# Kernel tuning notes

Hardware: AMD Instinct MI355X
Metric: run time of the kernel (lower is better)

The kernel has to match this reference:

```python
import jax, jax.numpy as jnp
import numpy as np

NUM_NODES = 100000
EMB_DIM = 256
HID_DIM = 256
NUM_REL = 500
NUM_EDGES = 250000


def setup_inputs() -> dict:
    key = jax.random.key(0)
    ks = jax.random.split(key, 6)
    x = jax.random.normal(ks[0], (NUM_NODES, EMB_DIM), dtype=jnp.float32)
    edge_index = jax.random.randint(ks[1], (2, NUM_EDGES), 0, NUM_NODES, dtype=jnp.int64)
    edge_type = jax.random.randint(ks[2], (NUM_EDGES,), 0, NUM_REL, dtype=jnp.int64)
    # nn.Linear weights: shape [out, in]; _init_weights -> normal(0,1), bias zero
    W_head = jax.random.normal(ks[3], (HID_DIM, EMB_DIM), dtype=jnp.float32)
    b_head = jnp.zeros((HID_DIM,), dtype=jnp.float32)
    W_tail = jax.random.normal(ks[4], (HID_DIM, EMB_DIM), dtype=jnp.float32)
    b_tail = jnp.zeros((HID_DIM,), dtype=jnp.float32)
    rel_emb = jax.random.normal(ks[5], (NUM_REL, HID_DIM), dtype=jnp.float32)
    return {"x": x, "edge_index": edge_index, "edge_type": edge_type,
            "W_head": W_head, "b_head": b_head,
            "W_tail": W_tail, "b_tail": b_tail, "rel_emb": rel_emb}


def reference(x, edge_index, edge_type, W_head, b_head, W_tail, b_tail, rel_emb):
    # gcn == 'no' branch of DistMultNet.forward
    h_head = x[edge_index[0]] @ W_head.T + b_head          # [E, H]
    h_tail = x[edge_index[1]] @ W_tail.T + b_tail          # [E, H]
    h_rel = rel_emb[edge_type]                             # [E, H]
    scores = jnp.sum(h_head * h_rel * h_tail, axis=1)      # [E]
    return jax.nn.sigmoid(scores)
```

## Files before the change

kernel.cpp:

```cpp
#include <hip/hip_runtime.h>
#include <math.h>

#define EMB 256

typedef _Float16 half8 __attribute__((ext_vector_type(8)));
typedef _Float16 half4v __attribute__((ext_vector_type(4)));
typedef float f32x4 __attribute__((ext_vector_type(4)));

__device__ __forceinline__ void split2(const float4 v, half4v& hi, half4v& lo) {
    hi[0] = (_Float16)v.x; hi[1] = (_Float16)v.y;
    hi[2] = (_Float16)v.z; hi[3] = (_Float16)v.w;
    lo[0] = (_Float16)(v.x - (float)hi[0]);
    lo[1] = (_Float16)(v.y - (float)hi[1]);
    lo[2] = (_Float16)(v.z - (float)hi[2]);
    lo[3] = (_Float16)(v.w - (float)hi[3]);
}

__global__ __launch_bounds__(256, 2)
void gemm_split_mfma(const float* __restrict__ X,
                     const float* __restrict__ Wh, const float* __restrict__ bh,
                     const float* __restrict__ Wt, const float* __restrict__ bt,
                     float* __restrict__ Hout, float* __restrict__ Tout, int M)
{
    __shared__ __align__(16) _Float16 Ab[128 * 64];
    __shared__ __align__(16) _Float16 Bb[128 * 64];

    const int tid = threadIdx.x;
    const int sel = blockIdx.x >> 1;
    const int n0  = (blockIdx.x & 1) << 7;
    const int m0  = blockIdx.y << 7;
    const float* __restrict__ Wsel = sel ? Wt : Wh;
    const float* __restrict__ bsel = sel ? bt : bh;
    float* __restrict__ OUT = sel ? Tout : Hout;

    const int lane = tid & 63;
    const int wv = tid >> 6;
    const int wm = (wv >> 1) << 6;
    const int wn = (wv & 1) << 6;
    const int l15 = lane & 15, l4 = lane >> 4;

    const int q    = tid & 7;
    const int srow = tid >> 3;
    const int ghi  = q >> 1;
    const int wby  = (q & 1) << 3;

    f32x4 acc[4][4];
#pragma unroll
    for (int i = 0; i < 4; ++i)
#pragma unroll
        for (int j = 0; j < 4; ++j) acc[i][j] = (f32x4){0.f, 0.f, 0.f, 0.f};

    float4 xg[4], wg[4];
#pragma unroll
    for (int p = 0; p < 4; ++p) {
        const int r = srow + p * 32;
        const int gm = m0 + r;
        xg[p] = (gm < M) ? *(const float4*)&X[(size_t)gm * EMB + q * 4]
                         : make_float4(0.f, 0.f, 0.f, 0.f);
        wg[p] = *(const float4*)&Wsel[(size_t)(n0 + r) * EMB + q * 4];
    }

    for (int k0 = 0; k0 < EMB; k0 += 32) {
        __syncthreads();
#pragma unroll
        for (int p = 0; p < 4; ++p) {
            const int r = srow + p * 32;
            const int r7 = r & 7;
            half4v hi, lo;
            split2(xg[p], hi, lo);
            char* abase = (char*)Ab + r * 128 + wby;
            *(half4v*)(abase + (((ghi    ) ^ r7) << 4)) = hi;
            *(half4v*)(abase + (((ghi + 4) ^ r7) << 4)) = lo;
            split2(wg[p], hi, lo);
            char* bbase = (char*)Bb + r * 128 + wby;
            *(half4v*)(bbase + (((ghi    ) ^ r7) << 4)) = hi;
            *(half4v*)(bbase + (((ghi + 4) ^ r7) << 4)) = lo;
        }
        __syncthreads();

        if (k0 + 32 < EMB) {
            const int kn = k0 + 32 + q * 4;
#pragma unroll
            for (int p = 0; p < 4; ++p) {
                const int r = srow + p * 32;
                const int gm = m0 + r;
                xg[p] = (gm < M) ? *(const float4*)&X[(size_t)gm * EMB + kn]
                                 : make_float4(0.f, 0.f, 0.f, 0.f);
                wg[p] = *(const float4*)&Wsel[(size_t)(n0 + r) * EMB + kn];
            }
        }

        half8 ah[4], al[4];
#pragma unroll
        for (int f = 0; f < 4; ++f) {
            const int m = wm + f * 16 + l15;
            const char* arow = (const char*)Ab + m * 128;
            ah[f] = *(const half8*)(arow + (((l4    ) ^ (m & 7)) << 4));
            al[f] = *(const half8*)(arow + (((l4 + 4) ^ (m & 7)) << 4));
        }
#pragma unroll
        for (int j = 0; j < 4; ++j) {
            const int n = wn + j * 16 + l15;
            const char* brow = (const char*)Bb + n * 128;
            const half8 bhv = *(const half8*)(brow + (((l4    ) ^ (n & 7)) << 4));
            const half8 blv = *(const half8*)(brow + (((l4 + 4) ^ (n & 7)) << 4));
#pragma unroll
            for (int i = 0; i < 4; ++i) {
                acc[i][j] = __builtin_amdgcn_mfma_f32_16x16x32_f16(ah[i], bhv, acc[i][j], 0, 0, 0);
                acc[i][j] = __builtin_amdgcn_mfma_f32_16x16x32_f16(ah[i], blv, acc[i][j], 0, 0, 0);
                acc[i][j] = __builtin_amdgcn_mfma_f32_16x16x32_f16(al[i], bhv, acc[i][j], 0, 0, 0);
            }
        }
    }

#pragma unroll
    for (int i = 0; i < 4; ++i) {
        const int rbase = m0 + wm + i * 16 + l4 * 4;
#pragma unroll
        for (int rg = 0; rg < 4; ++rg) {
            const int gr = rbase + rg;
            if (gr < M) {
                float* dst = &OUT[(size_t)gr * EMB + n0 + wn];
#pragma unroll
                for (int j = 0; j < 4; ++j) {
                    const int col = j * 16 + l15;
                    dst[col] = acc[i][j][rg] + bsel[n0 + wn + col];
                }
            }
        }
    }
}

__global__ __launch_bounds__(256)
void edge_score(const float* __restrict__ H, const float* __restrict__ T,
                const float* __restrict__ rel, const int* __restrict__ ei,
                const int* __restrict__ et, float* __restrict__ out, int E)
{
    const int lane = threadIdx.x & 63;
    const int wid = threadIdx.x >> 6;
    const int e = blockIdx.x * 4 + wid;
    if (e >= E) return;

    const int src = ei[e];
    const int dst = ei[E + e];
    const int r = et[e];

    const float4 h = *(const float4*)&H[(size_t)src * EMB + lane * 4];
    const float4 t = *(const float4*)&T[(size_t)dst * EMB + lane * 4];
    const float4 g = *(const float4*)&rel[(size_t)r * EMB + lane * 4];

    float s = h.x * g.x * t.x + h.y * g.y * t.y + h.z * g.z * t.z + h.w * g.w * t.w;
#pragma unroll
    for (int off = 32; off > 0; off >>= 1)
        s += __shfl_xor(s, off, 64);

    if (lane == 0) out[e] = 1.0f / (1.0f + expf(-s));
}

__global__ __launch_bounds__(256)
void edge_direct(const float* __restrict__ X, const int* __restrict__ ei,
                 const int* __restrict__ et,
                 const float* __restrict__ Wh, const float* __restrict__ bh,
                 const float* __restrict__ Wt, const float* __restrict__ bt,
                 const float* __restrict__ rel, float* __restrict__ out, int E)
{
    __shared__ float xsrc[EMB], xdst[EMB];
    __shared__ float red[256];
    const int e = blockIdx.x;
    const int tid = threadIdx.x;
    const int src = ei[e], dst = ei[E + e], r = et[e];

    xsrc[tid] = X[(size_t)src * EMB + tid];
    xdst[tid] = X[(size_t)dst * EMB + tid];
    __syncthreads();

    float ah = 0.f, at = 0.f;
    const float* wh = Wh + (size_t)tid * EMB;
    const float* wt = Wt + (size_t)tid * EMB;
#pragma unroll 8
    for (int k = 0; k < EMB; k += 4) {
        float4 w4 = *(const float4*)&wh[k];
        ah += w4.x * xsrc[k] + w4.y * xsrc[k + 1] + w4.z * xsrc[k + 2] + w4.w * xsrc[k + 3];
        float4 v4 = *(const float4*)&wt[k];
        at += v4.x * xdst[k] + v4.y * xdst[k + 1] + v4.z * xdst[k + 2] + v4.w * xdst[k + 3];
    }
    red[tid] = (ah + bh[tid]) * rel[(size_t)r * EMB + tid] * (at + bt[tid]);
    __syncthreads();
    for (int s2 = 128; s2 > 0; s2 >>= 1) {
        if (tid < s2) red[tid] += red[tid + s2];
        __syncthreads();
    }
    if (tid == 0) out[e] = 1.0f / (1.0f + expf(-red[0]));
}

extern "C" void kernel_launch(void* const* d_in, const int* in_sizes, int n_in,
                              void* d_out, int out_size, void* d_ws, size_t ws_size,
                              hipStream_t stream) {
    const float* x   = (const float*)d_in[0];
    const int*   ei  = (const int*)d_in[1];
    const int*   et  = (const int*)d_in[2];
    const float* Wh  = (const float*)d_in[3];
    const float* bh  = (const float*)d_in[4];
    const float* Wt  = (const float*)d_in[5];
    const float* bt  = (const float*)d_in[6];
    const float* rel = (const float*)d_in[7];
    float* out = (float*)d_out;

    const int M = in_sizes[0] / EMB;
    const int E = in_sizes[2];

    const size_t need = (size_t)2 * M * EMB * sizeof(float);
    if (ws_size >= need) {
        float* H = (float*)d_ws;
        float* T = H + (size_t)M * EMB;
        dim3 grid(4, (M + 127) / 128);
        gemm_split_mfma<<<grid, 256, 0, stream>>>(x, Wh, bh, Wt, bt, H, T, M);
        edge_score<<<(E + 3) / 4, 256, 0, stream>>>(H, T, rel, ei, et, out, E);
    } else {
        edge_direct<<<E, 256, 0, stream>>>(x, ei, et, Wh, bh, Wt, bt, rel, out, E);
    }
}
```

Measured before the change: 217.4 us.

## Pre-split inputs to hi/lo fp16 and stream GEMM tiles via global_load_lds

Adds a presplit kernel that converts X and both weight matrices once into swizzled hi/lo fp16 layouts in workspace. The GEMM then loads these tiles directly into LDS with global_load_lds, so the per-block fp32 loads and conversion work move out of the main loop. Previously every block recomputed the split of X for each of its four output tiles. The cost is an extra kernel launch plus writing and rereading an fp16 copy of X that is the same size as the fp32 original. The new GEMM also drops the register-prefetch software pipelining, so loads and MFMA work no longer overlap within a block.

```diff
diff --git a/kernel.cpp b/kernel.cpp
--- a/kernel.cpp
+++ b/kernel.cpp
@@ -4,9 +4,135 @@
 #define EMB 256
 
 typedef _Float16 half8 __attribute__((ext_vector_type(8)));
+typedef float f32x4 __attribute__((ext_vector_type(4)));
+
+__device__ __forceinline__ void gload_lds16(const void* gsrc, void* lds) {
+    __builtin_amdgcn_global_load_lds(
+        (const __attribute__((address_space(1))) void*)gsrc,
+        (__attribute__((address_space(3))) void*)lds,
+        16, 0, 0);
+}
+
+__global__ void presplit(const float* __restrict__ X,
+                         const float* __restrict__ Wh, const float* __restrict__ Wt,
+                         _Float16* __restrict__ Xs, _Float16* __restrict__ Whs,
+                         _Float16* __restrict__ Wts, int M)
+{
+    const int total = (M + 512) * 32;
+    for (int g = blockIdx.x * 256 + threadIdx.x; g < total; g += gridDim.x * 256) {
+        const int m = g >> 5;
+        const int cs = g & 31;
+        const int c = cs >> 2, seg = cs & 3;
+
+        const float* src; _Float16* dst; int r;
+        if (m < M)            { src = X;  dst = Xs;  r = m; }
+        else if (m < M + 256) { src = Wh; dst = Whs; r = m - M; }
+        else                  { src = Wt; dst = Wts; r = m - M - 256; }
+
+        const float* s = src + (size_t)r * EMB + c * 32 + seg * 8;
+        const float4 v0 = *(const float4*)s;
+        const float4 v1 = *(const float4*)(s + 4);
+        const float f[8] = {v0.x, v0.y, v0.z, v0.w, v1.x, v1.y, v1.z, v1.w};
+        half8 hi, lo;
+#pragma unroll
+        for (int i = 0; i < 8; ++i) {
+            hi[i] = (_Float16)f[i];
+            lo[i] = (_Float16)(f[i] - (float)hi[i]);
+        }
+        _Float16* d = dst + (size_t)r * 512 + c * 64;
+        const int sw = r & 7;
+        *(half8*)(d + ((seg     ^ sw) << 3)) = hi;
+        *(half8*)(d + (((4 + seg) ^ sw) << 3)) = lo;
+    }
+}
+
+__global__ __launch_bounds__(256, 2)
+void gemm_f16_3term(const _Float16* __restrict__ Xs,
+                    const _Float16* __restrict__ Whs, const _Float16* __restrict__ Wts,
+                    const float* __restrict__ bh, const float* __restrict__ bt,
+                    float* __restrict__ Hout, float* __restrict__ Tout, int M)
+{
+    __shared__ __align__(16) _Float16 Abuf[128 * 64];
+    __shared__ __align__(16) _Float16 Bbuf[128 * 64];
+
+    const int tid = threadIdx.x;
+    const int sel = blockIdx.x >> 1;
+    const int n0  = (blockIdx.x & 1) << 7;
+    const int m0  = blockIdx.y << 7;
+    const _Float16* __restrict__ Ws = sel ? Wts : Whs;
+    const float* __restrict__ bias  = sel ? bt : bh;
+    float* __restrict__ OUT         = sel ? Tout : Hout;
+
+    const int lane = tid & 63;
+    const int wv = tid >> 6;
+    const int wm = (wv >> 1) << 6;
+    const int wn = (wv & 1) << 6;
+    const int l15 = lane & 15, l4 = lane >> 4;
+
+    const int srow = tid >> 3;
+    const int sgr  = tid & 7;
+    const char* abase = (const char*)Xs + (size_t)m0 * 1024;
+    const char* bbase = (const char*)Ws + (size_t)n0 * 1024;
+
+    f32x4 acc[4][4];
+#pragma unroll
+    for (int i = 0; i < 4; ++i)
+#pragma unroll
+        for (int j = 0; j < 4; ++j) acc[i][j] = (f32x4){0.f, 0.f, 0.f, 0.f};
+
+    for (int c = 0; c < 8; ++c) {
+        if (c) __syncthreads();
+#pragma unroll
+        for (int i = 0; i < 4; ++i) {
+            const int row = i * 32 + srow;
+            const int off = row * 128 + sgr * 16;
+            gload_lds16(abase + (size_t)row * 1024 + c * 128 + sgr * 16, (char*)Abuf + off);
+            gload_lds16(bbase + (size_t)row * 1024 + c * 128 + sgr * 16, (char*)Bbuf + off);
+        }
+        __syncthreads();
+
+        half8 ah[4], al[4];
+#pragma unroll
+        for (int f = 0; f < 4; ++f) {
+            const int row = wm + f * 16 + l15;
+            const char* rb = (const char*)Abuf + row * 128;
+            ah[f] = *(const half8*)(rb + ((l4       ^ (row & 7)) << 4));
+            al[f] = *(const half8*)(rb + (((4 + l4) ^ (row & 7)) << 4));
+        }
+#pragma unroll
+        for (int j = 0; j < 4; ++j) {
+            const int n = wn + j * 16 + l15;
+            const char* rb = (const char*)Bbuf + n * 128;
+            const half8 bhf = *(const half8*)(rb + ((l4       ^ (n & 7)) << 4));
+            const half8 blf = *(const half8*)(rb + (((4 + l4) ^ (n & 7)) << 4));
+#pragma unroll
+            for (int i = 0; i < 4; ++i) {
+                acc[i][j] = __builtin_amdgcn_mfma_f32_16x16x32_f16(ah[i], bhf, acc[i][j], 0, 0, 0);
+                acc[i][j] = __builtin_amdgcn_mfma_f32_16x16x32_f16(ah[i], blf, acc[i][j], 0, 0, 0);
+                acc[i][j] = __builtin_amdgcn_mfma_f32_16x16x32_f16(al[i], bhf, acc[i][j], 0, 0, 0);
+            }
+        }
+    }
+
+#pragma unroll
+    for (int i = 0; i < 4; ++i) {
+        const int rbase = m0 + wm + i * 16 + l4 * 4;
+#pragma unroll
+        for (int rg = 0; rg < 4; ++rg) {
+            const int gr = rbase + rg;
+            if (gr < M) {
+                float* dst = &OUT[(size_t)gr * EMB + n0 + wn];
+#pragma unroll
+                for (int j = 0; j < 4; ++j) {
+                    const int col = j * 16 + l15;
+                    dst[col] = acc[i][j][rg] + bias[n0 + wn + col];
+                }
+            }
+        }
+    }
+}
+
 typedef _Float16 half4v __attribute__((ext_vector_type(4)));
-typedef float f32x4 __attribute__((ext_vector_type(4)));
-
 __device__ __forceinline__ void split2(const float4 v, half4v& hi, half4v& lo) {
     hi[0] = (_Float16)v.x; hi[1] = (_Float16)v.y;
     hi[2] = (_Float16)v.z; hi[3] = (_Float16)v.w;
@@ -68,13 +194,13 @@
             const int r7 = r & 7;
             half4v hi, lo;
             split2(xg[p], hi, lo);
-            char* abase = (char*)Ab + r * 128 + wby;
-            *(half4v*)(abase + (((ghi    ) ^ r7) << 4)) = hi;
-            *(half4v*)(abase + (((ghi + 4) ^ r7) << 4)) = lo;
+            char* ab = (char*)Ab + r * 128 + wby;
+            *(half4v*)(ab + (((ghi    ) ^ r7) << 4)) = hi;
+            *(half4v*)(ab + (((ghi + 4) ^ r7) << 4)) = lo;
             split2(wg[p], hi, lo);
-            char* bbase = (char*)Bb + r * 128 + wby;
-            *(half4v*)(bbase + (((ghi    ) ^ r7) << 4)) = hi;
-            *(half4v*)(bbase + (((ghi + 4) ^ r7) << 4)) = lo;
+            char* bb = (char*)Bb + r * 128 + wby;
+            *(half4v*)(bb + (((ghi    ) ^ r7) << 4)) = hi;
+            *(half4v*)(bb + (((ghi + 4) ^ r7) << 4)) = lo;
         }
         __syncthreads();
 
@@ -94,16 +220,16 @@
 #pragma unroll
         for (int f = 0; f < 4; ++f) {
             const int m = wm + f * 16 + l15;
-            const char* arow = (const char*)Ab + m * 128;
-            ah[f] = *(const half8*)(arow + (((l4    ) ^ (m & 7)) << 4));
-            al[f] = *(const half8*)(arow + (((l4 + 4) ^ (m & 7)) << 4));
+            const char* ar = (const char*)Ab + m * 128;
+            ah[f] = *(const half8*)(ar + (((l4    ) ^ (m & 7)) << 4));
+            al[f] = *(const half8*)(ar + (((l4 + 4) ^ (m & 7)) << 4));
         }
 #pragma unroll
         for (int j = 0; j < 4; ++j) {
             const int n = wn + j * 16 + l15;
-            const char* brow = (const char*)Bb + n * 128;
-            const half8 bhv = *(const half8*)(brow + (((l4    ) ^ (n & 7)) << 4));
-            const half8 blv = *(const half8*)(brow + (((l4 + 4) ^ (n & 7)) << 4));
+            const char* br = (const char*)Bb + n * 128;
+            const half8 bhv = *(const half8*)(br + (((l4    ) ^ (n & 7)) << 4));
+            const half8 blv = *(const half8*)(br + (((l4 + 4) ^ (n & 7)) << 4));
 #pragma unroll
             for (int i = 0; i < 4; ++i) {
                 acc[i][j] = __builtin_amdgcn_mfma_f32_16x16x32_f16(ah[i], bhv, acc[i][j], 0, 0, 0);
@@ -209,8 +335,23 @@
     const int M = in_sizes[0] / EMB;
     const int E = in_sizes[2];
 
-    const size_t need = (size_t)2 * M * EMB * sizeof(float);
-    if (ws_size >= need) {
+    const size_t szHT = (size_t)2 * M * EMB * sizeof(float);
+    const size_t szXs = (size_t)M * 512 * sizeof(_Float16);
+    const size_t szWs = (size_t)2 * 256 * 512 * sizeof(_Float16);
+    const size_t need_full = szHT + szXs + szWs;
+
+    if (ws_size >= need_full) {
+        float* H = (float*)d_ws;
+        float* T = H + (size_t)M * EMB;
+        _Float16* Xs  = (_Float16*)((char*)d_ws + szHT);
+        _Float16* Whs = Xs + (size_t)M * 512;
+        _Float16* Wts = Whs + (size_t)256 * 512;
+
+        presplit<<<2048, 256, 0, stream>>>(x, Wh, Wt, Xs, Whs, Wts, M);
+        dim3 grid(4, (M + 127) / 128);
+        gemm_f16_3term<<<grid, 256, 0, stream>>>(Xs, Whs, Wts, bh, bt, H, T, M);
+        edge_score<<<(E + 3) / 4, 256, 0, stream>>>(H, T, rel, ei, et, out, E);
+    } else if (ws_size >= szHT) {
         float* H = (float*)d_ws;
         float* T = H + (size_t)M * EMB;
         dim3 grid(4, (M + 127) / 128);
```

Measured after the change: 232.6 us. 7.0% more time.

## Fuse head/tail GEMMs sharing X tile, load via global_load_lds, XCD-aware remap

Applied to the files above, without the earlier changes.

The two projection GEMMs now run in one kernel. Each block loads its X tile once and computes both the head and tail outputs, which halves X reads. Tiles arrive in LDS as fp32 through direct global-to-LDS loads and are split into hi/lo fp16 when read from LDS, replacing the register-staged prefetch. Block IDs are remapped so adjacent tiles land on the same XCD for L2 locality. The cost is twice the accumulator registers, 48KB of LDS, and no overlap between the next load and the current compute, which may reduce occupancy.

```diff
diff --git a/kernel.cpp b/kernel.cpp
--- a/kernel.cpp
+++ b/kernel.cpp
@@ -4,115 +4,123 @@
 #define EMB 256
 
 typedef _Float16 half8 __attribute__((ext_vector_type(8)));
-typedef _Float16 half4v __attribute__((ext_vector_type(4)));
 typedef float f32x4 __attribute__((ext_vector_type(4)));
 
-__device__ __forceinline__ void split2(const float4 v, half4v& hi, half4v& lo) {
-    hi[0] = (_Float16)v.x; hi[1] = (_Float16)v.y;
-    hi[2] = (_Float16)v.z; hi[3] = (_Float16)v.w;
-    lo[0] = (_Float16)(v.x - (float)hi[0]);
-    lo[1] = (_Float16)(v.y - (float)hi[1]);
-    lo[2] = (_Float16)(v.z - (float)hi[2]);
-    lo[3] = (_Float16)(v.w - (float)hi[3]);
+__device__ __forceinline__ void gload_lds16(const void* gsrc, void* lds) {
+    __builtin_amdgcn_global_load_lds(
+        (const __attribute__((address_space(1))) void*)gsrc,
+        (__attribute__((address_space(3))) void*)lds,
+        16, 0, 0);
+}
+
+__device__ __forceinline__ void split8(const f32x4 a, const f32x4 b,
+                                       half8& hi, half8& lo) {
+#pragma unroll
+    for (int i = 0; i < 4; ++i) {
+        hi[i]     = (_Float16)a[i];
+        lo[i]     = (_Float16)(a[i] - (float)hi[i]);
+        hi[4 + i] = (_Float16)b[i];
+        lo[4 + i] = (_Float16)(b[i] - (float)hi[4 + i]);
+    }
 }
 
 __global__ __launch_bounds__(256, 2)
-void gemm_split_mfma(const float* __restrict__ X,
-                     const float* __restrict__ Wh, const float* __restrict__ bh,
-                     const float* __restrict__ Wt, const float* __restrict__ bt,
-                     float* __restrict__ Hout, float* __restrict__ Tout, int M)
+void gemm_dual(const float* __restrict__ X,
+               const float* __restrict__ Wh, const float* __restrict__ bh,
+               const float* __restrict__ Wt, const float* __restrict__ bt,
+               float* __restrict__ Hout, float* __restrict__ Tout,
+               int M, int nwg)
 {
-    __shared__ __align__(16) _Float16 Ab[128 * 64];
-    __shared__ __align__(16) _Float16 Bb[128 * 64];
+    __shared__ __align__(16) float Af [128 * 32];
+    __shared__ __align__(16) float Bhf[128 * 32];
+    __shared__ __align__(16) float Btf[128 * 32];
+
+    const int fl = blockIdx.x;
+    const int q = nwg >> 3, r = nwg & 7;
+    const int xcd = fl & 7, ix = fl >> 3;
+    const int wg = (xcd < r) ? xcd * (q + 1) + ix
+                             : r * (q + 1) + (xcd - r) * q + ix;
+    const int n0 = (wg & 1) << 7;
+    const int m0 = (wg >> 1) << 7;
 
     const int tid = threadIdx.x;
-    const int sel = blockIdx.x >> 1;
-    const int n0  = (blockIdx.x & 1) << 7;
-    const int m0  = blockIdx.y << 7;
-    const float* __restrict__ Wsel = sel ? Wt : Wh;
-    const float* __restrict__ bsel = sel ? bt : bh;
-    float* __restrict__ OUT = sel ? Tout : Hout;
-
     const int lane = tid & 63;
     const int wv = tid >> 6;
     const int wm = (wv >> 1) << 6;
     const int wn = (wv & 1) << 6;
     const int l15 = lane & 15, l4 = lane >> 4;
 
-    const int q    = tid & 7;
+    const int s  = l15 & 7;
+    const int ga = (((l4 << 1) ^ s) << 4);
+    const int gb = ga ^ 16;
+
     const int srow = tid >> 3;
-    const int ghi  = q >> 1;
-    const int wby  = (q & 1) << 3;
-
-    f32x4 acc[4][4];
+    const int sg   = tid & 7;
+    const int swg  = (sg ^ (srow & 7)) << 4;
+    const int sldo = srow * 128 + sg * 16;
+
+    f32x4 accH[4][4], accT[4][4];
 #pragma unroll
     for (int i = 0; i < 4; ++i)
 #pragma unroll
-        for (int j = 0; j < 4; ++j) acc[i][j] = (f32x4){0.f, 0.f, 0.f, 0.f};
-
-    float4 xg[4], wg[4];
-#pragma unroll
-    for (int p = 0; p < 4; ++p) {
-        const int r = srow + p * 32;
-        const int gm = m0 + r;
-        xg[p] = (gm < M) ? *(const float4*)&X[(size_t)gm * EMB + q * 4]
-                         : make_float4(0.f, 0.f, 0.f, 0.f);
-        wg[p] = *(const float4*)&Wsel[(size_t)(n0 + r) * EMB + q * 4];
-    }
-
-    for (int k0 = 0; k0 < EMB; k0 += 32) {
+        for (int j = 0; j < 4; ++j) {
+            accH[i][j] = (f32x4){0.f, 0.f, 0.f, 0.f};
+            accT[i][j] = (f32x4){0.f, 0.f, 0.f, 0.f};
+        }
+
+    for (int c = 0; c < 8; ++c) {
+        if (c) __syncthreads();
+        const int cb = c << 7;
+#pragma unroll
+        for (int i = 0; i < 4; ++i) {
+            const int row = srow + (i << 5);
+            const int gm = m0 + row;
+            const int gmc = gm < M ? gm : M - 1;
+            const int ldso = sldo + (i << 12);
+            gload_lds16((const char*)X  + (size_t)gmc * 1024 + cb + swg,
+                        (char*)Af + ldso);
+            gload_lds16((const char*)Wh + (size_t)(n0 + row) * 1024 + cb + swg,
+                        (char*)Bhf + ldso);
+            gload_lds16((const char*)Wt + (size_t)(n0 + row) * 1024 + cb + swg,
+                        (char*)Btf + ldso);
+        }
         __syncthreads();
-#pragma unroll
-        for (int p = 0; p < 4; ++p) {
-            const int r = srow + p * 32;
-            const int r7 = r & 7;
-            half4v hi, lo;
-            split2(xg[p], hi, lo);
-            char* abase = (char*)Ab + r * 128 + wby;
-            *(half4v*)(abase + (((ghi    ) ^ r7) << 4)) = hi;
-            *(half4v*)(abase + (((ghi + 4) ^ r7) << 4)) = lo;
-            split2(wg[p], hi, lo);
-            char* bbase = (char*)Bb + r * 128 + wby;
-            *(half4v*)(bbase + (((ghi    ) ^ r7) << 4)) = hi;
-            *(half4v*)(bbase + (((ghi + 4) ^ r7) << 4)) = lo;
-        }
-        __syncthreads();
-
-        if (k0 + 32 < EMB) {
-            const int kn = k0 + 32 + q * 4;
-#pragma unroll
-            for (int p = 0; p < 4; ++p) {
-                const int r = srow + p * 32;
-                const int gm = m0 + r;
-                xg[p] = (gm < M) ? *(const float4*)&X[(size_t)gm * EMB + kn]
-                                 : make_float4(0.f, 0.f, 0.f, 0.f);
-                wg[p] = *(const float4*)&Wsel[(size_t)(n0 + r) * EMB + kn];
+
+        half8 ahh[4], ahl[4];
+#pragma unroll
+        for (int fi = 0; fi < 4; ++fi) {
+            const char* ar = (const char*)Af + (wm + fi * 16 + l15) * 128;
+            split8(*(const f32x4*)(ar + ga), *(const f32x4*)(ar + gb),
+                   ahh[fi], ahl[fi]);
+        }
+#pragma unroll
+        for (int j = 0; j < 4; ++j) {
+            const int nrow = (wn + j * 16 + l15) * 128;
+            half8 bhh, bhl, bth, btl;
+            {
+                const char* hr = (const char*)Bhf + nrow;
+                split8(*(const f32x4*)(hr + ga), *(const f32x4*)(hr + gb), bhh, bhl);
+                const char* tr = (const char*)Btf + nrow;
+                split8(*(const f32x4*)(tr + ga), *(const f32x4*)(tr + gb), bth, btl);
             }
-        }
-
-        half8 ah[4], al[4];
-#pragma unroll
-        for (int f = 0; f < 4; ++f) {
-            const int m = wm + f * 16 + l15;
-            const char* arow = (const char*)Ab + m * 128;
-            ah[f] = *(const half8*)(arow + (((l4    ) ^ (m & 7)) << 4));
-            al[f] = *(const half8*)(arow + (((l4 + 4) ^ (m & 7)) << 4));
-        }
-#pragma unroll
-        for (int j = 0; j < 4; ++j) {
-            const int n = wn + j * 16 + l15;
-            const char* brow = (const char*)Bb + n * 128;
-            const half8 bhv = *(const half8*)(brow + (((l4    ) ^ (n & 7)) << 4));
-            const half8 blv = *(const half8*)(brow + (((l4 + 4) ^ (n & 7)) << 4));
 #pragma unroll
             for (int i = 0; i < 4; ++i) {
-                acc[i][j] = __builtin_amdgcn_mfma_f32_16x16x32_f16(ah[i], bhv, acc[i][j], 0, 0, 0);
-                acc[i][j] = __builtin_amdgcn_mfma_f32_16x16x32_f16(ah[i], blv, acc[i][j], 0, 0, 0);
-                acc[i][j] = __builtin_amdgcn_mfma_f32_16x16x32_f16(al[i], bhv, acc[i][j], 0, 0, 0);
+                accH[i][j] = __builtin_amdgcn_mfma_f32_16x16x32_f16(ahh[i], bhh, accH[i][j], 0, 0, 0);
+                accH[i][j] = __builtin_amdgcn_mfma_f32_16x16x32_f16(ahh[i], bhl, accH[i][j], 0, 0, 0);
+                accH[i][j] = __builtin_amdgcn_mfma_f32_16x16x32_f16(ahl[i], bhh, accH[i][j], 0, 0, 0);
+                accT[i][j] = __builtin_amdgcn_mfma_f32_16x16x32_f16(ahh[i], bth, accT[i][j], 0, 0, 0);
+                accT[i][j] = __builtin_amdgcn_mfma_f32_16x16x32_f16(ahh[i], btl, accT[i][j], 0, 0, 0);
+                accT[i][j] = __builtin_amdgcn_mfma_f32_16x16x32_f16(ahl[i], bth, accT[i][j], 0, 0, 0);
             }
         }
     }
 
+    float bhv[4], btv[4];
+#pragma unroll
+    for (int j = 0; j < 4; ++j) {
+        bhv[j] = bh[n0 + wn + j * 16 + l15];
+        btv[j] = bt[n0 + wn + j * 16 + l15];
+    }
 #pragma unroll
     for (int i = 0; i < 4; ++i) {
         const int rbase = m0 + wm + i * 16 + l4 * 4;
@@ -120,11 +128,13 @@
         for (int rg = 0; rg < 4; ++rg) {
             const int gr = rbase + rg;
             if (gr < M) {
-                float* dst = &OUT[(size_t)gr * EMB + n0 + wn];
+                float* dh = &Hout[(size_t)gr * EMB + n0 + wn];
+                float* dt = &Tout[(size_t)gr * EMB + n0 + wn];
 #pragma unroll
                 for (int j = 0; j < 4; ++j) {
                     const int col = j * 16 + l15;
-                    dst[col] = acc[i][j][rg] + bsel[n0 + wn + col];
+                    dh[col] = accH[i][j][rg] + bhv[j];
+                    dt[col] = accT[i][j][rg] + btv[j];
                 }
             }
         }
@@ -209,12 +219,14 @@
     const int M = in_sizes[0] / EMB;
     const int E = in_sizes[2];
 
-    const size_t need = (size_t)2 * M * EMB * sizeof(float);
-    if (ws_size >= need) {
+    const size_t szHT = (size_t)2 * M * EMB * sizeof(float);
+
+    if (ws_size >= szHT) {
         float* H = (float*)d_ws;
         float* T = H + (size_t)M * EMB;
-        dim3 grid(4, (M + 127) / 128);
-        gemm_split_mfma<<<grid, 256, 0, stream>>>(x, Wh, bh, Wt, bt, H, T, M);
+        const int mtiles = (M + 127) / 128;
+        const int nwg = 2 * mtiles;
+        gemm_dual<<<nwg, 256, 0, stream>>>(x, Wh, bh, Wt, bt, H, T, M, nwg);
         edge_score<<<(E + 3) / 4, 256, 0, stream>>>(H, T, rel, ei, et, out, E);
     } else {
         edge_direct<<<E, 256, 0, stream>>>(x, ei, et, Wh, bh, Wt, bt, rel, out, E);
```

Result: faster. 204.6 us (-5.9%).
